# Kernel optimization log

Measured on AMD Instinct MI355X. Metric: run time of the kernel, lower is better.

## Reference

```python
import jax, jax.numpy as jnp
import numpy as np

B, S, D, F, E = 4, 2048, 1024, 4096, 8
LN_EPS = 1e-5


def setup_inputs() -> dict:
    key = jax.random.key(0)
    ks = jax.random.split(key, 6)
    sc = 0.02
    return {
        "x": jax.random.normal(ks[0], (B, S, D), dtype=jnp.float32),
        "Wr": jax.random.normal(ks[1], (D, E), dtype=jnp.float32) * sc,
        "br": jnp.zeros((E,), jnp.float32),
        "ln_g": jnp.ones((D,), jnp.float32),
        "ln_b": jnp.zeros((D,), jnp.float32),
        "W1": jax.random.normal(ks[2], (E, D, F), dtype=jnp.float32) * sc,
        "b1": jnp.zeros((E, F), jnp.float32),
        "W2": jax.random.normal(ks[3], (E, F, D), dtype=jnp.float32) * sc,
        "b2": jnp.zeros((E, D), jnp.float32),
    }


def reference(x, Wr, br, ln_g, ln_b, W1, b1, W2, b2):
    tokens_shape = x.shape[:-1]
    xt = x.reshape(-1, x.shape[-1])  # [T, D]

    # top-1 routing (eval mode: no jitter noise, no dropout)
    router_logits = xt @ Wr + br                      # [T, E]
    router_probs = jax.nn.softmax(router_logits, axis=-1)
    gates = jnp.max(router_probs, axis=-1, keepdims=True)   # [T, 1]
    idx = jnp.argmax(router_probs, axis=-1)                 # [T] int
    onehot = jax.nn.one_hot(idx, E, dtype=xt.dtype)         # [T, E]

    # layernorm
    mu = jnp.mean(xt, axis=-1, keepdims=True)
    var = jnp.mean(jnp.square(xt - mu), axis=-1, keepdims=True)
    xn = (xt - mu) * jax.lax.rsqrt(var + LN_EPS) * ln_g + ln_b

    # expert FFN: per-token expert-specific GEMMs expressed via one-hot dispatch
    h = jnp.einsum('te,td,edf->tf', onehot, xn, W1) + b1[idx]  # [T, F]
    h = jax.nn.relu(h)
    y = jnp.einsum('te,tf,efd->td', onehot, h, W2) + b2[idx]   # [T, D]

    y = y * gates
    return y.reshape(tokens_shape + (y.shape[-1],))
```

## Files before the change

kernel.cpp:

```cpp
#include <hip/hip_runtime.h>
#include <stdint.h>

#define T_TOK 8192
#define DDIM  1024
#define FDIM  4096
#define NEXP  8
#define BM 128
#define BN 128
#define BK 32
#define MAX_MT (T_TOK / BM + NEXP)

typedef __attribute__((ext_vector_type(8))) short bf16x8;
typedef __attribute__((ext_vector_type(8))) unsigned short u16x8;
typedef __attribute__((ext_vector_type(4))) float f32x4;

__device__ __forceinline__ unsigned short f2bf(float f) {
    union { float f; unsigned u; } v; v.f = f;
    unsigned u = v.u;
    u += 0x7fffu + ((u >> 16) & 1u);
    return (unsigned short)(u >> 16);
}

__device__ __forceinline__ void async16(const void* g, void* l) {
    __builtin_amdgcn_global_load_lds(
        (const __attribute__((address_space(1))) unsigned int*)g,
        (__attribute__((address_space(3))) unsigned int*)l, 16, 0, 0);
}

__global__ __launch_bounds__(256) void transpose_bf16(
    const float* __restrict__ src, unsigned short* __restrict__ dst, int R, int C) {
    __shared__ float tile[64][65];
    int e = blockIdx.z;
    int c0 = blockIdx.x * 64, r0 = blockIdx.y * 64;
    const float* s = src + (size_t)e * R * C;
    unsigned short* d = dst + (size_t)e * R * C;
    int tid = threadIdx.x;
    int lr = tid >> 4;
    int lc = (tid & 15) * 4;
#pragma unroll
    for (int i = 0; i < 4; i++) {
        float4 v = *(const float4*)&s[(size_t)(r0 + lr + i * 16) * C + c0 + lc];
        tile[lr + i * 16][lc + 0] = v.x;
        tile[lr + i * 16][lc + 1] = v.y;
        tile[lr + i * 16][lc + 2] = v.z;
        tile[lr + i * 16][lc + 3] = v.w;
    }
    __syncthreads();
#pragma unroll
    for (int i = 0; i < 2; i++) {
        int idx = tid + i * 256;
        int drow = idx >> 3;
        int seg  = idx & 7;
        u16x8 o;
#pragma unroll
        for (int j = 0; j < 8; j++) o[j] = f2bf(tile[seg * 8 + j][drow]);
        *(u16x8*)&d[(size_t)(c0 + drow) * R + r0 + seg * 8] = o;
    }
}

__global__ __launch_bounds__(256) void router_ln(
    const float* __restrict__ x, const float* __restrict__ Wr, const float* __restrict__ br,
    const float* __restrict__ lng, const float* __restrict__ lnb,
    unsigned short* __restrict__ xn, float* __restrict__ gate,
    int* __restrict__ expert, int* __restrict__ counts) {
    int t = blockIdx.x, tid = threadIdx.x;
    const float4* xv4 = (const float4*)(x + (size_t)t * DDIM);
    float4 xv = xv4[tid];
    float s  = xv.x + xv.y + xv.z + xv.w;
    float sq = xv.x * xv.x + xv.y * xv.y + xv.z * xv.z + xv.w * xv.w;
    float lg[8] = {0, 0, 0, 0, 0, 0, 0, 0};
    const float4* wr4 = (const float4*)Wr;
    int d0 = tid * 4;
    const float* xr = (const float*)&xv;
#pragma unroll
    for (int r = 0; r < 4; r++) {
        float4 w0 = wr4[(d0 + r) * 2];
        float4 w1 = wr4[(d0 + r) * 2 + 1];
        lg[0] += xr[r] * w0.x; lg[1] += xr[r] * w0.y; lg[2] += xr[r] * w0.z; lg[3] += xr[r] * w0.w;
        lg[4] += xr[r] * w1.x; lg[5] += xr[r] * w1.y; lg[6] += xr[r] * w1.z; lg[7] += xr[r] * w1.w;
    }
#pragma unroll
    for (int o = 32; o > 0; o >>= 1) {
        s += __shfl_down(s, o); sq += __shfl_down(sq, o);
#pragma unroll
        for (int e = 0; e < 8; e++) lg[e] += __shfl_down(lg[e], o);
    }
    __shared__ float red[4][10];
    __shared__ float bc[2];
    int lane = tid & 63, wv = tid >> 6;
    if (lane == 0) {
        red[wv][0] = s; red[wv][1] = sq;
#pragma unroll
        for (int e = 0; e < 8; e++) red[wv][2 + e] = lg[e];
    }
    __syncthreads();
    if (tid == 0) {
        float S = 0, SQ = 0, L[8] = {0, 0, 0, 0, 0, 0, 0, 0};
        for (int w = 0; w < 4; w++) {
            S += red[w][0]; SQ += red[w][1];
            for (int e = 0; e < 8; e++) L[e] += red[w][2 + e];
        }
        float mu = S * (1.f / DDIM);
        float var = SQ * (1.f / DDIM) - mu * mu;
        float rstd = rsqrtf(var + 1e-5f);
        int best = 0; float bl = -3.4e38f;
        for (int e = 0; e < 8; e++) {
            float l = L[e] + br[e];
            L[e] = l;
            if (l > bl) { bl = l; best = e; }
        }
        float den = 0;
        for (int e = 0; e < 8; e++) den += __expf(L[e] - bl);
        gate[t] = 1.f / den;
        expert[t] = best;
        atomicAdd(&counts[best], 1);
        bc[0] = mu; bc[1] = rstd;
    }
    __syncthreads();
    float mu = bc[0], rstd = bc[1];
    float4 gg = ((const float4*)lng)[tid];
    float4 bb = ((const float4*)lnb)[tid];
    ushort4 o;
    o.x = f2bf((xv.x - mu) * rstd * gg.x + bb.x);
    o.y = f2bf((xv.y - mu) * rstd * gg.y + bb.y);
    o.z = f2bf((xv.z - mu) * rstd * gg.z + bb.z);
    o.w = f2bf((xv.w - mu) * rstd * gg.w + bb.w);
    *(ushort4*)(xn + (size_t)t * DDIM + d0) = o;
}

__global__ __launch_bounds__(256) void scatter_perm(
    const int* __restrict__ expert, const int* __restrict__ counts,
    int* __restrict__ fill, int* __restrict__ perm) {
    __shared__ int offs_s[NEXP];
    if (threadIdx.x < NEXP) {
        int o = 0;
        for (int i = 0; i < (int)threadIdx.x; i++) o += counts[i];
        offs_s[threadIdx.x] = o;
    }
    __syncthreads();
    int t = blockIdx.x * 256 + threadIdx.x;
    int e = expert[t];
    int p = atomicAdd(&fill[e], 1);
    perm[offs_s[e] + p] = t;
}

template <int MODE>
__global__ __launch_bounds__(256) void gemm_grouped(
    const unsigned short* __restrict__ A, const unsigned short* __restrict__ Bt,
    const float* __restrict__ bias, unsigned short* __restrict__ Hout,
    float* __restrict__ Yout, const float* __restrict__ gate,
    const int* __restrict__ perm, const int* __restrict__ counts,
    int K, int N) {
    int rem = blockIdx.x;
    int e, off = 0, cnt = 0; bool found = false;
    for (e = 0; e < NEXP; e++) {
        cnt = counts[e];
        int mt = (cnt + (BM - 1)) >> 7;
        if (rem < mt) { found = true; break; }
        rem -= mt; off += cnt;
    }
    if (!found) return;
    int mbase = rem << 7;
    int mrem = cnt - mbase;
    int n0 = blockIdx.y << 7;

    __shared__ __align__(16) unsigned short Alds[BM * BK];
    __shared__ __align__(16) unsigned short Blds[BN * BK];

    int tid = threadIdx.x;
    int lane = tid & 63, wave = tid >> 6;
    int grow = lane >> 2;
    int seg  = lane & 3;

    const unsigned short* ag[2];
    const unsigned short* bg[2];
    unsigned short* al[2];
    unsigned short* bl[2];
#pragma unroll
    for (int p = 0; p < 2; p++) {
        int r = p * 64 + wave * 16 + grow;
        int rr = (r < mrem) ? r : 0;
        int t = perm[off + mbase + rr];
        ag[p] = A + (size_t)t * K + seg * 8;
        bg[p] = Bt + ((size_t)e * N + n0 + r) * K + seg * 8;
        al[p] = &Alds[(p * 64 + wave * 16) * BK];
        bl[p] = &Blds[(p * 64 + wave * 16) * BK];
    }

    int wr = (wave >> 1) * 64, wc = (wave & 1) * 64;
    int q = lane >> 4, l16 = lane & 15;

    f32x4 acc[4][4] = {};

    for (int k0 = 0; k0 < K; k0 += BK) {
#pragma unroll
        for (int p = 0; p < 2; p++) {
            async16(ag[p] + k0, al[p]);
            async16(bg[p] + k0, bl[p]);
        }
        __syncthreads();
        bf16x8 af[4], bfr[4];
#pragma unroll
        for (int i = 0; i < 4; i++)
            af[i] = *(const bf16x8*)&Alds[(wr + i * 16 + l16) * BK + q * 8];
#pragma unroll
        for (int j = 0; j < 4; j++)
            bfr[j] = *(const bf16x8*)&Blds[(wc + j * 16 + l16) * BK + q * 8];
#pragma unroll
        for (int i = 0; i < 4; i++)
#pragma unroll
            for (int j = 0; j < 4; j++)
                acc[i][j] = __builtin_amdgcn_mfma_f32_16x16x32_bf16(af[i], bfr[j], acc[i][j], 0, 0, 0);
        __syncthreads();
    }

    float bs[4];
#pragma unroll
    for (int j = 0; j < 4; j++) bs[j] = bias[(size_t)e * N + n0 + wc + j * 16 + l16];
#pragma unroll
    for (int i = 0; i < 4; i++) {
#pragma unroll
        for (int r = 0; r < 4; r++) {
            int lrow = wr + i * 16 + q * 4 + r;
            if (lrow < mrem) {
                int t = perm[off + mbase + lrow];
                if (MODE == 0) {
                    unsigned short* hp = Hout + (size_t)t * N + n0 + wc + l16;
#pragma unroll
                    for (int j = 0; j < 4; j++) {
                        float v = acc[i][j][r] + bs[j];
                        hp[j * 16] = f2bf(fmaxf(v, 0.f));
                    }
                } else {
                    float gt = gate[t];
                    float* yp = Yout + (size_t)t * N + n0 + wc + l16;
#pragma unroll
                    for (int j = 0; j < 4; j++)
                        yp[j * 16] = (acc[i][j][r] + bs[j]) * gt;
                }
            }
        }
    }
}

extern "C" void kernel_launch(void* const* d_in, const int* in_sizes, int n_in,
                              void* d_out, int out_size, void* d_ws, size_t ws_size,
                              hipStream_t stream) {
    const float* x   = (const float*)d_in[0];
    const float* Wr  = (const float*)d_in[1];
    const float* br  = (const float*)d_in[2];
    const float* lng = (const float*)d_in[3];
    const float* lnb = (const float*)d_in[4];
    const float* W1  = (const float*)d_in[5];
    const float* b1  = (const float*)d_in[6];
    const float* W2  = (const float*)d_in[7];
    const float* b2  = (const float*)d_in[8];
    float* out = (float*)d_out;

    char* ws = (char*)d_ws;
    size_t o = 0;
    unsigned short* W1t = (unsigned short*)(ws + o); o += (size_t)NEXP * DDIM * FDIM * 2;
    unsigned short* W2t = (unsigned short*)(ws + o); o += (size_t)NEXP * DDIM * FDIM * 2;
    unsigned short* xn  = (unsigned short*)(ws + o); o += (size_t)T_TOK * DDIM * 2;
    unsigned short* h   = (unsigned short*)(ws + o); o += (size_t)T_TOK * FDIM * 2;
    float* gate = (float*)(ws + o); o += (size_t)T_TOK * 4;
    int* expert = (int*)(ws + o);   o += (size_t)T_TOK * 4;
    int* perm   = (int*)(ws + o);   o += (size_t)T_TOK * 4;
    int* meta   = (int*)(ws + o);
    int* counts = meta;
    int* fill   = meta + 8;

    hipMemsetAsync(meta, 0, 16 * sizeof(int), stream);

    transpose_bf16<<<dim3(FDIM / 64, DDIM / 64, NEXP), 256, 0, stream>>>(W1, W1t, DDIM, FDIM);
    transpose_bf16<<<dim3(DDIM / 64, FDIM / 64, NEXP), 256, 0, stream>>>(W2, W2t, FDIM, DDIM);
    router_ln<<<T_TOK, 256, 0, stream>>>(x, Wr, br, lng, lnb, xn, gate, expert, counts);
    scatter_perm<<<T_TOK / 256, 256, 0, stream>>>(expert, counts, fill, perm);
    gemm_grouped<0><<<dim3(MAX_MT, FDIM / BN), 256, 0, stream>>>(
        xn, W1t, b1, h, nullptr, nullptr, perm, counts, DDIM, FDIM);
    gemm_grouped<1><<<dim3(MAX_MT, DDIM / BN), 256, 0, stream>>>(
        h, W2t, b2, nullptr, out, gate, perm, counts, FDIM, DDIM);
}
```

Baseline: 746.1 us.

## Fuse weight transposes into router kernel, store h in sorted order, narrow GEMM2 tiles

Merges the two weight-transpose kernels and the router/layernorm kernel into one launch that picks its work from the block index, cutting launch gaps and letting the pieces overlap. The first GEMM now writes h in expert-sorted row order, so the second GEMM reads A rows contiguously instead of gathering them through perm. The second GEMM uses 128x64 tiles to double its block count, since its N is only 1024. Smaller tiles lower per-block data reuse, and the fused prep kernel's shared-memory footprint is set by the transpose path.

After: 714.4 us. -4.2%, faster.

```diff
diff --git a/kernel.cpp b/kernel.cpp
--- a/kernel.cpp
+++ b/kernel.cpp
@@ -6,7 +6,6 @@
 #define FDIM  4096
 #define NEXP  8
 #define BM 128
-#define BN 128
 #define BK 32
 #define MAX_MT (T_TOK / BM + NEXP)
 
@@ -27,43 +26,57 @@
         (__attribute__((address_space(3))) unsigned int*)l, 16, 0, 0);
 }
 
-__global__ __launch_bounds__(256) void transpose_bf16(
-    const float* __restrict__ src, unsigned short* __restrict__ dst, int R, int C) {
-    __shared__ float tile[64][65];
-    int e = blockIdx.z;
-    int c0 = blockIdx.x * 64, r0 = blockIdx.y * 64;
-    const float* s = src + (size_t)e * R * C;
-    unsigned short* d = dst + (size_t)e * R * C;
-    int tid = threadIdx.x;
-    int lr = tid >> 4;
-    int lc = (tid & 15) * 4;
-#pragma unroll
-    for (int i = 0; i < 4; i++) {
-        float4 v = *(const float4*)&s[(size_t)(r0 + lr + i * 16) * C + c0 + lc];
-        tile[lr + i * 16][lc + 0] = v.x;
-        tile[lr + i * 16][lc + 1] = v.y;
-        tile[lr + i * 16][lc + 2] = v.z;
-        tile[lr + i * 16][lc + 3] = v.w;
-    }
-    __syncthreads();
-#pragma unroll
-    for (int i = 0; i < 2; i++) {
-        int idx = tid + i * 256;
-        int drow = idx >> 3;
-        int seg  = idx & 7;
-        u16x8 o;
-#pragma unroll
-        for (int j = 0; j < 8; j++) o[j] = f2bf(tile[seg * 8 + j][drow]);
-        *(u16x8*)&d[(size_t)(c0 + drow) * R + r0 + seg * 8] = o;
-    }
-}
-
-__global__ __launch_bounds__(256) void router_ln(
+__global__ __launch_bounds__(256) void prep(
     const float* __restrict__ x, const float* __restrict__ Wr, const float* __restrict__ br,
     const float* __restrict__ lng, const float* __restrict__ lnb,
-    unsigned short* __restrict__ xn, float* __restrict__ gate,
+    const float* __restrict__ W1, const float* __restrict__ W2,
+    unsigned short* __restrict__ xn, unsigned short* __restrict__ W1t,
+    unsigned short* __restrict__ W2t, float* __restrict__ gate,
     int* __restrict__ expert, int* __restrict__ counts) {
-    int t = blockIdx.x, tid = threadIdx.x;
+    __shared__ float smem[64 * 65];
+    int b = blockIdx.x, tid = threadIdx.x;
+
+    if (b >= T_TOK) {
+        int idx = b - T_TOK;
+        const float* src; unsigned short* dst; int R, C, e, c0, r0;
+        if (idx < 8192) {
+            R = DDIM; C = FDIM;
+            e = idx >> 10;
+            c0 = (idx & 63) * 64; r0 = ((idx >> 6) & 15) * 64;
+            src = W1; dst = W1t;
+        } else {
+            idx -= 8192;
+            R = FDIM; C = DDIM;
+            e = idx >> 10;
+            c0 = (idx & 15) * 64; r0 = ((idx >> 4) & 63) * 64;
+            src = W2; dst = W2t;
+        }
+        const float* s = src + (size_t)e * R * C;
+        unsigned short* d = dst + (size_t)e * R * C;
+        float (*tile)[65] = (float(*)[65])smem;
+        int lr = tid >> 4, lc = (tid & 15) * 4;
+#pragma unroll
+        for (int i = 0; i < 4; i++) {
+            float4 v = *(const float4*)&s[(size_t)(r0 + lr + i * 16) * C + c0 + lc];
+            tile[lr + i * 16][lc + 0] = v.x;
+            tile[lr + i * 16][lc + 1] = v.y;
+            tile[lr + i * 16][lc + 2] = v.z;
+            tile[lr + i * 16][lc + 3] = v.w;
+        }
+        __syncthreads();
+#pragma unroll
+        for (int i = 0; i < 2; i++) {
+            int ix = tid + i * 256;
+            int drow = ix >> 3, seg = ix & 7;
+            u16x8 o;
+#pragma unroll
+            for (int j = 0; j < 8; j++) o[j] = f2bf(tile[seg * 8 + j][drow]);
+            *(u16x8*)&d[(size_t)(c0 + drow) * R + r0 + seg * 8] = o;
+        }
+        return;
+    }
+
+    int t = b;
     const float4* xv4 = (const float4*)(x + (size_t)t * DDIM);
     float4 xv = xv4[tid];
     float s  = xv.x + xv.y + xv.z + xv.w;
@@ -85,20 +98,20 @@
 #pragma unroll
         for (int e = 0; e < 8; e++) lg[e] += __shfl_down(lg[e], o);
     }
-    __shared__ float red[4][10];
-    __shared__ float bc[2];
+    float* red = smem;
+    float* bc = smem + 40;
     int lane = tid & 63, wv = tid >> 6;
     if (lane == 0) {
-        red[wv][0] = s; red[wv][1] = sq;
-#pragma unroll
-        for (int e = 0; e < 8; e++) red[wv][2 + e] = lg[e];
+        red[wv * 10 + 0] = s; red[wv * 10 + 1] = sq;
+#pragma unroll
+        for (int e = 0; e < 8; e++) red[wv * 10 + 2 + e] = lg[e];
     }
     __syncthreads();
     if (tid == 0) {
         float S = 0, SQ = 0, L[8] = {0, 0, 0, 0, 0, 0, 0, 0};
         for (int w = 0; w < 4; w++) {
-            S += red[w][0]; SQ += red[w][1];
-            for (int e = 0; e < 8; e++) L[e] += red[w][2 + e];
+            S += red[w * 10 + 0]; SQ += red[w * 10 + 1];
+            for (int e = 0; e < 8; e++) L[e] += red[w * 10 + 2 + e];
         }
         float mu = S * (1.f / DDIM);
         float var = SQ * (1.f / DDIM) - mu * mu;
@@ -151,6 +164,10 @@
     float* __restrict__ Yout, const float* __restrict__ gate,
     const int* __restrict__ perm, const int* __restrict__ counts,
     int K, int N) {
+    constexpr int BN_ = (MODE == 0) ? 128 : 64;
+    constexpr int AI  = (MODE == 0) ? 4 : 2;
+    constexpr int BROWS = (MODE == 0) ? 2 : 1;
+
     int rem = blockIdx.x;
     int e, off = 0, cnt = 0; bool found = false;
     for (e = 0; e < NEXP; e++) {
@@ -162,10 +179,10 @@
     if (!found) return;
     int mbase = rem << 7;
     int mrem = cnt - mbase;
-    int n0 = blockIdx.y << 7;
+    int n0 = blockIdx.y * BN_;
 
     __shared__ __align__(16) unsigned short Alds[BM * BK];
-    __shared__ __align__(16) unsigned short Blds[BN * BK];
+    __shared__ __align__(16) unsigned short Blds[BN_ * BK];
 
     int tid = threadIdx.x;
     int lane = tid & 63, wave = tid >> 6;
@@ -173,41 +190,49 @@
     int seg  = lane & 3;
 
     const unsigned short* ag[2];
-    const unsigned short* bg[2];
     unsigned short* al[2];
-    unsigned short* bl[2];
+    const unsigned short* bg[BROWS];
+    unsigned short* bl[BROWS];
 #pragma unroll
     for (int p = 0; p < 2; p++) {
         int r = p * 64 + wave * 16 + grow;
         int rr = (r < mrem) ? r : 0;
-        int t = perm[off + mbase + rr];
-        ag[p] = A + (size_t)t * K + seg * 8;
+        if (MODE == 0) {
+            int t = perm[off + mbase + rr];
+            ag[p] = A + (size_t)t * K + seg * 8;
+        } else {
+            ag[p] = A + (size_t)(off + mbase + rr) * K + seg * 8;
+        }
+        al[p] = &Alds[(p * 64 + wave * 16) * BK];
+    }
+#pragma unroll
+    for (int p = 0; p < BROWS; p++) {
+        int r = p * 64 + wave * 16 + grow;
         bg[p] = Bt + ((size_t)e * N + n0 + r) * K + seg * 8;
-        al[p] = &Alds[(p * 64 + wave * 16) * BK];
         bl[p] = &Blds[(p * 64 + wave * 16) * BK];
     }
 
-    int wr = (wave >> 1) * 64, wc = (wave & 1) * 64;
+    int wr = (MODE == 0) ? (wave >> 1) * 64 : wave * 32;
+    int wc = (MODE == 0) ? (wave & 1) * 64 : 0;
     int q = lane >> 4, l16 = lane & 15;
 
-    f32x4 acc[4][4] = {};
+    f32x4 acc[AI][4] = {};
 
     for (int k0 = 0; k0 < K; k0 += BK) {
 #pragma unroll
-        for (int p = 0; p < 2; p++) {
-            async16(ag[p] + k0, al[p]);
-            async16(bg[p] + k0, bl[p]);
-        }
+        for (int p = 0; p < 2; p++) async16(ag[p] + k0, al[p]);
+#pragma unroll
+        for (int p = 0; p < BROWS; p++) async16(bg[p] + k0, bl[p]);
         __syncthreads();
-        bf16x8 af[4], bfr[4];
-#pragma unroll
-        for (int i = 0; i < 4; i++)
+        bf16x8 af[AI], bfr[4];
+#pragma unroll
+        for (int i = 0; i < AI; i++)
             af[i] = *(const bf16x8*)&Alds[(wr + i * 16 + l16) * BK + q * 8];
 #pragma unroll
         for (int j = 0; j < 4; j++)
             bfr[j] = *(const bf16x8*)&Blds[(wc + j * 16 + l16) * BK + q * 8];
 #pragma unroll
-        for (int i = 0; i < 4; i++)
+        for (int i = 0; i < AI; i++)
 #pragma unroll
             for (int j = 0; j < 4; j++)
                 acc[i][j] = __builtin_amdgcn_mfma_f32_16x16x32_bf16(af[i], bfr[j], acc[i][j], 0, 0, 0);
@@ -218,20 +243,20 @@
 #pragma unroll
     for (int j = 0; j < 4; j++) bs[j] = bias[(size_t)e * N + n0 + wc + j * 16 + l16];
 #pragma unroll
-    for (int i = 0; i < 4; i++) {
+    for (int i = 0; i < AI; i++) {
 #pragma unroll
         for (int r = 0; r < 4; r++) {
             int lrow = wr + i * 16 + q * 4 + r;
             if (lrow < mrem) {
-                int t = perm[off + mbase + lrow];
                 if (MODE == 0) {
-                    unsigned short* hp = Hout + (size_t)t * N + n0 + wc + l16;
+                    unsigned short* hp = Hout + (size_t)(off + mbase + lrow) * N + n0 + wc + l16;
 #pragma unroll
                     for (int j = 0; j < 4; j++) {
                         float v = acc[i][j][r] + bs[j];
                         hp[j * 16] = f2bf(fmaxf(v, 0.f));
                     }
                 } else {
+                    int t = perm[off + mbase + lrow];
                     float gt = gate[t];
                     float* yp = Yout + (size_t)t * N + n0 + wc + l16;
 #pragma unroll
@@ -272,12 +297,11 @@
 
     hipMemsetAsync(meta, 0, 16 * sizeof(int), stream);
 
-    transpose_bf16<<<dim3(FDIM / 64, DDIM / 64, NEXP), 256, 0, stream>>>(W1, W1t, DDIM, FDIM);
-    transpose_bf16<<<dim3(DDIM / 64, FDIM / 64, NEXP), 256, 0, stream>>>(W2, W2t, FDIM, DDIM);
-    router_ln<<<T_TOK, 256, 0, stream>>>(x, Wr, br, lng, lnb, xn, gate, expert, counts);
+    prep<<<T_TOK + 16384, 256, 0, stream>>>(x, Wr, br, lng, lnb, W1, W2,
+                                            xn, W1t, W2t, gate, expert, counts);
     scatter_perm<<<T_TOK / 256, 256, 0, stream>>>(expert, counts, fill, perm);
-    gemm_grouped<0><<<dim3(MAX_MT, FDIM / BN), 256, 0, stream>>>(
+    gemm_grouped<0><<<dim3(MAX_MT, FDIM / 128), 256, 0, stream>>>(
         xn, W1t, b1, h, nullptr, nullptr, perm, counts, DDIM, FDIM);
-    gemm_grouped<1><<<dim3(MAX_MT, DDIM / BN), 256, 0, stream>>>(
+    gemm_grouped<1><<<dim3(MAX_MT, DDIM / 64), 256, 0, stream>>>(
         h, W2t, b2, nullptr, out, gate, perm, counts, FDIM, DDIM);
 }
```
